# Kernel tuning notes

Hardware: AMD Instinct MI355X
Metric: run time of the kernel (lower is better)

## Reference

```python
import jax, jax.numpy as jnp
import numpy as np
from jax import lax

EPS = 1e-5
N_CROPS = 501
CROP_W = 500
RF = 65          # temporal receptive field
KS = 15          # conv1 kernel size
POOL = 3


def _bn(x, g, b, m, v, axis=1):
    shp = [1] * x.ndim
    shp[axis] = -1
    inv = g.reshape(shp) / jnp.sqrt(v.reshape(shp) + EPS)
    return (x - m.reshape(shp)) * inv + b.reshape(shp)


def setup_inputs() -> dict:
    key = jax.random.key(0)
    ks = jax.random.split(key, 16)
    B, C_IN, CH, T = 16, 1, 22, 1001
    F = 36
    OUT = 4
    FLAT = F * 43  # 1548 (corrected fc in_features; repo constant 504 is inconsistent)
    d = {
        "x": jax.random.normal(ks[0], (B, C_IN, CH, T), jnp.float32),
        # temporal conv [1,65]
        "w_t": jax.random.normal(ks[1], (F, 1, 1, RF), jnp.float32) * 0.1,
        "b_t": jax.random.normal(ks[2], (F,), jnp.float32) * 0.1,
        "bn_t_g": jax.random.uniform(ks[3], (F,), jnp.float32, 0.5, 1.5),
        "bn_t_b": jax.random.normal(ks[4], (F,), jnp.float32) * 0.1,
        "bn_t_m": jax.random.normal(ks[5], (F,), jnp.float32) * 0.1,
        "bn_t_v": jax.random.uniform(ks[6], (F,), jnp.float32, 0.5, 1.5),
        # spatial conv [22,1]
        "w_s": jax.random.normal(ks[7], (F, F, CH, 1), jnp.float32) * 0.05,
        "b_s": jax.random.normal(ks[8], (F,), jnp.float32) * 0.1,
        "bn_s_g": jax.random.uniform(ks[9], (F,), jnp.float32, 0.5, 1.5),
        "bn_s_b": jax.random.normal(ks[10], (F,), jnp.float32) * 0.1,
        "bn_s_m": jax.random.normal(ks[11], (F,), jnp.float32) * 0.1,
        "bn_s_v": jax.random.uniform(ks[12], (F,), jnp.float32, 0.5, 1.5),
        # conv1 [1,15] (as 1-D conv over time)
        "w_c": jax.random.normal(ks[13], (F, F, KS), jnp.float32) * 0.05,
        "b_c": jax.random.normal(ks[14], (F,), jnp.float32) * 0.1,
        "bn_c_g": jnp.ones((F,), jnp.float32),
        "bn_c_b": jnp.zeros((F,), jnp.float32),
        "bn_c_m": jnp.zeros((F,), jnp.float32),
        "bn_c_v": jnp.ones((F,), jnp.float32),
        # fc
        "w_fc": jax.random.normal(ks[15], (OUT, FLAT), jnp.float32) * 0.02,
        "b_fc": jnp.zeros((OUT,), jnp.float32),
    }
    return d


def reference(x, w_t, b_t, bn_t_g, bn_t_b, bn_t_m, bn_t_v,
              w_s, b_s, bn_s_g, bn_s_b, bn_s_m, bn_s_v,
              w_c, b_c, bn_c_g, bn_c_b, bn_c_m, bn_c_v,
              w_fc, b_fc):
    B = x.shape[0]
    F = w_t.shape[0]
    OUT = b_fc.shape[0]

    # temporal + spatial conv/BN/ELU are shift-invariant -> compute once over full T
    h = lax.conv_general_dilated(x, w_t, (1, 1), 'VALID',
                                 dimension_numbers=('NCHW', 'OIHW', 'NCHW'))
    h = h + b_t[None, :, None, None]                       # [B,36,22,937]
    h = jax.nn.elu(_bn(h, bn_t_g, bn_t_b, bn_t_m, bn_t_v))
    h = lax.conv_general_dilated(h, w_s, (1, 1), 'VALID',
                                 dimension_numbers=('NCHW', 'OIHW', 'NCHW'))
    h = h + b_s[None, :, None, None]                       # [B,36,1,937]
    h = jax.nn.elu(_bn(h, bn_s_g, bn_s_b, bn_s_m, bn_s_v))
    h = h[:, :, 0, :]                                      # [B,36,937]

    TW = CROP_W - RF + 1  # 436: temporal width of each crop after temporal conv

    def crop_logits(i):
        sl = lax.dynamic_slice_in_dim(h, i, TW, axis=2)    # [B,36,436]
        p1 = sl[:, :, :435].reshape(B, F, 145, POOL).mean(-1)  # avgpool1 -> [B,36,145]
        c = lax.conv_general_dilated(p1, w_c, (1,), 'VALID',
                                     dimension_numbers=('NCH', 'OIH', 'NCH'))
        c = c + b_c[None, :, None]                          # [B,36,131]
        c = jax.nn.elu(_bn(c, bn_c_g, bn_c_b, bn_c_m, bn_c_v))
        p2 = c[:, :, :129].reshape(B, F, 43, POOL).mean(-1)  # avgpool2 -> [B,36,43]
        flat = p2.reshape(B, -1)                            # [B,1548]
        return flat @ w_fc.T + b_fc                         # [B,OUT]

    def step(acc, i):
        return acc + crop_logits(i), None

    init = jnp.zeros((B, OUT), x.dtype)
    total, _ = lax.scan(step, init, jnp.arange(N_CROPS))
    return total / N_CROPS
```

## Files before the change

### kernel.cpp

```cpp
#include <hip/hip_runtime.h>

#define EPS 1e-5f
#define B 16
#define CH 22
#define T_IN 1001
#define F 36
#define RF 65
#define T1 937
#define FC 792
#define KW 99
#define UN 885
#define PSPAN 304
#define KS 15
#define GN 295
#define WN 129
#define M43 43
#define BF 576
#define FLAT 1548

#define H2_OFF  0
#define EP_OFF  539712
#define WTT_OFF 4617792
#define WST_OFF 4620132
#define WCT_OFF 4648644
#define BN_OFF  4668084
#define H1_OFF  4668352

__device__ __forceinline__ float elu_f(float v) {
    return v > 0.f ? v : (__expf(v) - 1.f);
}

__global__ __launch_bounds__(256) void k_prep(
    const float* __restrict__ w_t, const float* __restrict__ w_s,
    const float* __restrict__ w_c,
    const float* __restrict__ b_t, const float* __restrict__ g_t,
    const float* __restrict__ be_t,const float* __restrict__ m_t,
    const float* __restrict__ v_t,
    const float* __restrict__ b_s, const float* __restrict__ g_s,
    const float* __restrict__ be_s,const float* __restrict__ m_s,
    const float* __restrict__ v_s,
    const float* __restrict__ b_c, const float* __restrict__ g_c,
    const float* __restrict__ be_c,const float* __restrict__ m_c,
    const float* __restrict__ v_c, const float* __restrict__ b_fc,
    float* __restrict__ wtT, float* __restrict__ wsT,
    float* __restrict__ wcT, float* __restrict__ bnz,
    float* __restrict__ out)
{
    int i = blockIdx.x * 256 + threadIdx.x;
    if (i < F * RF)     { int k = i / F,  fi = i % F; wtT[i] = w_t[fi * RF + k]; }
    if (i < FC * F)     { int fc = i / F, fo = i % F; wsT[i] = w_s[fo * FC + fc]; }
    if (i < F * KS * F) { int fk = i / F, fo = i % F; int f = fk / KS, k = fk % KS;
                          wcT[i] = w_c[(fo * F + f) * KS + k]; }
    if (i < F) {
        float s1 = g_t[i] * rsqrtf(v_t[i] + EPS);
        bnz[i]          = s1;
        bnz[F + i]      = (b_t[i] - m_t[i]) * s1 + be_t[i];
        float s2 = g_s[i] * rsqrtf(v_s[i] + EPS);
        bnz[2 * F + i]  = s2;
        bnz[3 * F + i]  = (b_s[i] - m_s[i]) * s2 + be_s[i];
        float s3 = g_c[i] * rsqrtf(v_c[i] + EPS);
        bnz[4 * F + i]  = s3;
        bnz[5 * F + i]  = (b_c[i] - m_c[i]) * s3 + be_c[i];
    }
    if (i < B * 4) out[i] = b_fc[i & 3];
}

__global__ __launch_bounds__(256) void k_tconv(
    const float* __restrict__ x, const float* __restrict__ wtT,
    const float* __restrict__ bnz, float* __restrict__ h1,
    int t_base, int TS, int TSeff)
{
    const int tloc = blockIdx.x * 256 + threadIdx.x;
    const int b = blockIdx.z, ch = blockIdx.y;
    int t = t_base + tloc;
    int tc = t < (T1 - 1) ? t : (T1 - 1);
    const float* xp = x + (b * CH + ch) * T_IN + tc;

    float acc[F];
    #pragma unroll
    for (int j = 0; j < F; ++j) acc[j] = 0.f;

    #pragma unroll 4
    for (int kk = 0; kk < 16; ++kk) {
        float4 xv4 = *(const float4*)(xp + 4 * kk);
        const float* wr0 = wtT + (4 * kk + 0) * F;
        const float* wr1 = wtT + (4 * kk + 1) * F;
        const float* wr2 = wtT + (4 * kk + 2) * F;
        const float* wr3 = wtT + (4 * kk + 3) * F;
        #pragma unroll
        for (int j = 0; j < F; ++j) {
            acc[j] += xv4.x * wr0[j];
            acc[j] += xv4.y * wr1[j];
            acc[j] += xv4.z * wr2[j];
            acc[j] += xv4.w * wr3[j];
        }
    }
    {
        float xv = xp[64];
        const float* wr = wtT + 64 * F;
        #pragma unroll
        for (int j = 0; j < F; ++j) acc[j] += xv * wr[j];
    }

    if (t < T1 && tloc < TSeff) {
        #pragma unroll
        for (int j = 0; j < F; ++j) {
            float s1 = bnz[j], o1 = bnz[F + j];
            h1[((size_t)(b * F + j) * CH + ch) * TS + tloc] =
                elu_f(acc[j] * s1 + o1);
        }
    }
}

__global__ __launch_bounds__(512) void k_sconv(
    const float* __restrict__ h1, const float* __restrict__ wsT,
    const float* __restrict__ bnz, float* __restrict__ h2,
    int t_base, int TS, int TSeff)
{
    __shared__ float Ls[8 * F * 64];
    const int tid = threadIdx.x;
    const int lane = tid & 63;
    const int w = __builtin_amdgcn_readfirstlane(tid >> 6);
    const int b = blockIdx.y;
    const int tl0 = blockIdx.x * 64;
    int tl = tl0 + lane;
    int tlc = tl < (TSeff - 1) ? tl : (TSeff - 1);

    const float* hq = h1 + ((size_t)b * FC + w * KW) * TS + tlc;
    const float* wb = wsT + (w * KW) * F;

    float acc[F];
    #pragma unroll
    for (int j = 0; j < F; ++j) acc[j] = 0.f;

    #pragma unroll 11
    for (int fc = 0; fc < KW; ++fc) {
        float hv = hq[(size_t)fc * TS];
        const float* wr = wb + fc * F;
        #pragma unroll
        for (int j = 0; j < F; ++j) acc[j] += hv * wr[j];
    }

    #pragma unroll
    for (int j = 0; j < F; ++j) Ls[(w * F + j) * 64 + lane] = acc[j];
    __syncthreads();

    for (int i = tid; i < F * 64; i += 512) {
        float s = 0.f;
        #pragma unroll
        for (int wq = 0; wq < 8; ++wq) s += Ls[wq * (F * 64) + i];
        int fo = i >> 6;
        int tloc2 = tl0 + (i & 63);
        int tg = t_base + tloc2;
        if (tloc2 < TSeff) {
            float s2 = bnz[2 * F + fo], o2 = bnz[3 * F + fo];
            h2[(b * F + fo) * T1 + tg] = elu_f(s * s2 + o2);
        }
    }
}

__global__ __launch_bounds__(256) void k_qconv(
    const float* __restrict__ h2, const float* __restrict__ wcT,
    float* __restrict__ Ep)
{
    __shared__ float Ps[5 * PSPAN];
    const int tid = threadIdx.x;
    const int slice = blockIdx.y, b = blockIdx.z;
    const int u0 = blockIdx.x * 256;
    const int f_base = slice < 4 ? slice * 5 : 20 + (slice - 4) * 4;
    const int nf     = slice < 4 ? 5 : 4;

    for (int i = tid; i < nf * PSPAN; i += 256) {
        int fl = i / PSPAN, j = i % PSPAN;
        const float* hr = h2 + (size_t)(b * F + f_base + fl) * T1;
        int s = u0 + j;
        int s0 = s     < T1 - 1 ? s     : T1 - 1;
        int s1 = s + 1 < T1 - 1 ? s + 1 : T1 - 1;
        int s2 = s + 2 < T1 - 1 ? s + 2 : T1 - 1;
        Ps[i] = (hr[s0] + hr[s1] + hr[s2]) * (1.f / 3.f);
    }
    __syncthreads();

    const int lu = tid;

    float acc[F];
    #pragma unroll
    for (int j = 0; j < F; ++j) acc[j] = 0.f;

    for (int fl = 0; fl < nf; ++fl) {
        const int pb = fl * PSPAN + lu;
        #pragma unroll 5
        for (int k = 0; k < KS; ++k) {
            float pv = Ps[pb + 3 * k];
            const float* wr = wcT + ((f_base + fl) * KS + k) * F;
            #pragma unroll
            for (int j = 0; j < F; ++j) acc[j] += pv * wr[j];
        }
    }

    int u_g = u0 + lu;
    if (u_g < UN) {
        #pragma unroll
        for (int j = 0; j < F; ++j)
            Ep[(((size_t)slice * B + b) * F + j) * UN + u_g] = acc[j];
    }
}

__global__ __launch_bounds__(256) void k_wins(
    const float* __restrict__ Ep, const float* __restrict__ bnz,
    const float* __restrict__ w_fc, float* __restrict__ out)
{
    __shared__ float Es[UN];
    __shared__ float G[GN];
    __shared__ float Ws[WN];
    __shared__ float Sm[M43];
    const int tid = threadIdx.x;
    const int bf = blockIdx.x;
    const int b = bf / F, f = bf % F;
    const float sc = bnz[4 * F + f];
    const float oc = bnz[5 * F + f];
    for (int i = tid; i < UN; i += 256) {
        float s = 0.f;
        #pragma unroll
        for (int sl = 0; sl < 8; ++sl)
            s += Ep[((size_t)sl * BF + bf) * UN + i];
        Es[i] = elu_f(s * sc + oc);
    }
    __syncthreads();
    for (int q = tid; q < GN; q += 256)
        G[q] = Es[3 * q] + Es[3 * q + 1] + Es[3 * q + 2];
    __syncthreads();
    if (tid < WN) {
        float a = 0.f;
        for (int q = tid; q < tid + 167; ++q) a += G[q];
        Ws[tid] = a;
    }
    __syncthreads();
    if (tid < M43)
        Sm[tid] = (Ws[3 * tid] + Ws[3 * tid + 1] + Ws[3 * tid + 2]) * (1.f / 3.f);
    __syncthreads();
    if (tid < 4) {
        const float* wr = w_fc + tid * FLAT + f * M43;
        float a = 0.f;
        #pragma unroll 43
        for (int m = 0; m < M43; ++m) a += Sm[m] * wr[m];
        atomicAdd(&out[b * 4 + tid], a * (1.f / 501.f));
    }
}

extern "C" void kernel_launch(void* const* d_in, const int* in_sizes, int n_in,
                              void* d_out, int out_size, void* d_ws, size_t ws_size,
                              hipStream_t stream) {
    const float* x    = (const float*)d_in[0];
    const float* w_t  = (const float*)d_in[1];
    const float* b_t  = (const float*)d_in[2];
    const float* g_t  = (const float*)d_in[3];
    const float* be_t = (const float*)d_in[4];
    const float* m_t  = (const float*)d_in[5];
    const float* v_t  = (const float*)d_in[6];
    const float* w_s  = (const float*)d_in[7];
    const float* b_s  = (const float*)d_in[8];
    const float* g_s  = (const float*)d_in[9];
    const float* be_s = (const float*)d_in[10];
    const float* m_s  = (const float*)d_in[11];
    const float* v_s  = (const float*)d_in[12];
    const float* w_c  = (const float*)d_in[13];
    const float* b_c  = (const float*)d_in[14];
    const float* g_c  = (const float*)d_in[15];
    const float* be_c = (const float*)d_in[16];
    const float* m_c  = (const float*)d_in[17];
    const float* v_c  = (const float*)d_in[18];
    const float* w_fc = (const float*)d_in[19];
    const float* b_fc = (const float*)d_in[20];

    float* ws  = (float*)d_ws;
    float* h2  = ws + H2_OFF;
    float* Ep  = ws + EP_OFF;
    float* wtT = ws + WTT_OFF;
    float* wsT = ws + WST_OFF;
    float* wcT = ws + WCT_OFF;
    float* bnz = ws + BN_OFF;
    float* h1  = ws + H1_OFF;
    float* out = (float*)d_out;

    long long availF = (long long)(ws_size / 4) - (long long)H1_OFF;
    long long tsl = availF / (B * FC);
    int TS;
    if (tsl >= T1) TS = T1;
    else { TS = (int)(tsl & ~63LL); if (TS < 64) TS = 64; }
    int nslab = (T1 + TS - 1) / TS;

    k_prep<<<dim3(112), 256, 0, stream>>>(
        w_t, w_s, w_c, b_t, g_t, be_t, m_t, v_t,
        b_s, g_s, be_s, m_s, v_s, b_c, g_c, be_c, m_c, v_c, b_fc,
        wtT, wsT, wcT, bnz, out);

    for (int sl = 0; sl < nslab; ++sl) {
        int t_base = sl * TS;
        int TSeff = T1 - t_base; if (TSeff > TS) TSeff = TS;
        k_tconv<<<dim3((TSeff + 255) / 256, CH, B), 256, 0, stream>>>(
            x, wtT, bnz, h1, t_base, TS, TSeff);
        k_sconv<<<dim3((TSeff + 63) / 64, B), 512, 0, stream>>>(
            h1, wsT, bnz, h2, t_base, TS, TSeff);
    }

    k_qconv<<<dim3(4, 8, B), 256, 0, stream>>>(h2, wcT, Ep);
    k_wins<<<dim3(BF), 256, 0, stream>>>(Ep, bnz, w_fc, out);
}
```

Before: 176.4 us.

## Store temporal-conv intermediate as fp16 and split qconv by output channel

```diff
diff --git a/kernel.cpp b/kernel.cpp
--- a/kernel.cpp
+++ b/kernel.cpp
@@ -1,4 +1,5 @@
 #include <hip/hip_runtime.h>
+#include <hip/hip_fp16.h>
 
 #define EPS 1e-5f
 #define B 16
@@ -19,12 +20,12 @@
 #define FLAT 1548
 
 #define H2_OFF  0
-#define EP_OFF  539712
-#define WTT_OFF 4617792
-#define WST_OFF 4620132
-#define WCT_OFF 4648644
-#define BN_OFF  4668084
-#define H1_OFF  4668352
+#define E_OFF   539712
+#define WTT_OFF 1049472
+#define WST_OFF 1051812
+#define WCP_OFF 1080324
+#define BN_OFF  1101924
+#define H1_OFF  1102144
 
 __device__ __forceinline__ float elu_f(float v) {
     return v > 0.f ? v : (__expf(v) - 1.f);
@@ -43,14 +44,18 @@
     const float* __restrict__ be_c,const float* __restrict__ m_c,
     const float* __restrict__ v_c, const float* __restrict__ b_fc,
     float* __restrict__ wtT, float* __restrict__ wsT,
-    float* __restrict__ wcT, float* __restrict__ bnz,
+    float* __restrict__ wcP, float* __restrict__ bnz,
     float* __restrict__ out)
 {
     int i = blockIdx.x * 256 + threadIdx.x;
     if (i < F * RF)     { int k = i / F,  fi = i % F; wtT[i] = w_t[fi * RF + k]; }
     if (i < FC * F)     { int fc = i / F, fo = i % F; wsT[i] = w_s[fo * FC + fc]; }
-    if (i < F * KS * F) { int fk = i / F, fo = i % F; int f = fk / KS, k = fk % KS;
-                          wcT[i] = w_c[(fo * F + f) * KS + k]; }
+    if (i < 8 * F * KS * 5) {
+        int jj = i % 5, k = (i / 5) % KS, f = (i / (5 * KS)) % F, g = i / (5 * KS * F);
+        int fo = (g < 4 ? 5 * g : 20 + 4 * (g - 4)) + jj;
+        if (fo > F - 1) fo = F - 1;
+        wcP[i] = w_c[((size_t)fo * F + f) * KS + k];
+    }
     if (i < F) {
         float s1 = g_t[i] * rsqrtf(v_t[i] + EPS);
         bnz[i]          = s1;
@@ -67,7 +72,7 @@
 
 __global__ __launch_bounds__(256) void k_tconv(
     const float* __restrict__ x, const float* __restrict__ wtT,
-    const float* __restrict__ bnz, float* __restrict__ h1,
+    const float* __restrict__ bnz, __half* __restrict__ h1,
     int t_base, int TS, int TSeff)
 {
     const int tloc = blockIdx.x * 256 + threadIdx.x;
@@ -107,13 +112,13 @@
         for (int j = 0; j < F; ++j) {
             float s1 = bnz[j], o1 = bnz[F + j];
             h1[((size_t)(b * F + j) * CH + ch) * TS + tloc] =
-                elu_f(acc[j] * s1 + o1);
+                __float2half(elu_f(acc[j] * s1 + o1));
         }
     }
 }
 
 __global__ __launch_bounds__(512) void k_sconv(
-    const float* __restrict__ h1, const float* __restrict__ wsT,
+    const __half* __restrict__ h1, const float* __restrict__ wsT,
     const float* __restrict__ bnz, float* __restrict__ h2,
     int t_base, int TS, int TSeff)
 {
@@ -126,7 +131,7 @@
     int tl = tl0 + lane;
     int tlc = tl < (TSeff - 1) ? tl : (TSeff - 1);
 
-    const float* hq = h1 + ((size_t)b * FC + w * KW) * TS + tlc;
+    const __half* hq = h1 + ((size_t)b * FC + w * KW) * TS + tlc;
     const float* wb = wsT + (w * KW) * F;
 
     float acc[F];
@@ -135,7 +140,7 @@
 
     #pragma unroll 11
     for (int fc = 0; fc < KW; ++fc) {
-        float hv = hq[(size_t)fc * TS];
+        float hv = __half2float(hq[(size_t)fc * TS]);
         const float* wr = wb + fc * F;
         #pragma unroll
         for (int j = 0; j < F; ++j) acc[j] += hv * wr[j];
@@ -160,19 +165,19 @@
 }
 
 __global__ __launch_bounds__(256) void k_qconv(
-    const float* __restrict__ h2, const float* __restrict__ wcT,
-    float* __restrict__ Ep)
-{
-    __shared__ float Ps[5 * PSPAN];
+    const float* __restrict__ h2, const float* __restrict__ wcP,
+    const float* __restrict__ bnz, float* __restrict__ E)
+{
+    __shared__ float Ps[F * PSPAN];
     const int tid = threadIdx.x;
-    const int slice = blockIdx.y, b = blockIdx.z;
+    const int g = blockIdx.y, b = blockIdx.z;
     const int u0 = blockIdx.x * 256;
-    const int f_base = slice < 4 ? slice * 5 : 20 + (slice - 4) * 4;
-    const int nf     = slice < 4 ? 5 : 4;
-
-    for (int i = tid; i < nf * PSPAN; i += 256) {
+    const int fo0 = g < 4 ? g * 5 : 20 + (g - 4) * 4;
+    const int nfo = g < 4 ? 5 : 4;
+
+    for (int i = tid; i < F * PSPAN; i += 256) {
         int fl = i / PSPAN, j = i % PSPAN;
-        const float* hr = h2 + (size_t)(b * F + f_base + fl) * T1;
+        const float* hr = h2 + (size_t)(b * F + fl) * T1;
         int s = u0 + j;
         int s0 = s     < T1 - 1 ? s     : T1 - 1;
         int s1 = s + 1 < T1 - 1 ? s + 1 : T1 - 1;
@@ -181,34 +186,38 @@
     }
     __syncthreads();
 
-    const int lu = tid;
-
-    float acc[F];
+    float acc[5];
     #pragma unroll
-    for (int j = 0; j < F; ++j) acc[j] = 0.f;
-
-    for (int fl = 0; fl < nf; ++fl) {
-        const int pb = fl * PSPAN + lu;
+    for (int jj = 0; jj < 5; ++jj) acc[jj] = 0.f;
+
+    for (int f = 0; f < F; ++f) {
+        const int pb = f * PSPAN + tid;
+        const float* wf = wcP + (size_t)(g * F + f) * (KS * 5);
         #pragma unroll 5
         for (int k = 0; k < KS; ++k) {
             float pv = Ps[pb + 3 * k];
-            const float* wr = wcT + ((f_base + fl) * KS + k) * F;
+            const float* wr = wf + k * 5;
             #pragma unroll
-            for (int j = 0; j < F; ++j) acc[j] += pv * wr[j];
-        }
-    }
-
-    int u_g = u0 + lu;
+            for (int jj = 0; jj < 5; ++jj) acc[jj] += pv * wr[jj];
+        }
+    }
+
+    int u_g = u0 + tid;
     if (u_g < UN) {
         #pragma unroll
-        for (int j = 0; j < F; ++j)
-            Ep[(((size_t)slice * B + b) * F + j) * UN + u_g] = acc[j];
+        for (int jj = 0; jj < 5; ++jj) {
+            if (jj < nfo) {
+                int fo = fo0 + jj;
+                float sc = bnz[4 * F + fo], oc = bnz[5 * F + fo];
+                E[(size_t)(b * F + fo) * UN + u_g] = elu_f(acc[jj] * sc + oc);
+            }
+        }
     }
 }
 
 __global__ __launch_bounds__(256) void k_wins(
-    const float* __restrict__ Ep, const float* __restrict__ bnz,
-    const float* __restrict__ w_fc, float* __restrict__ out)
+    const float* __restrict__ E, const float* __restrict__ w_fc,
+    float* __restrict__ out)
 {
     __shared__ float Es[UN];
     __shared__ float G[GN];
@@ -217,15 +226,8 @@
     const int tid = threadIdx.x;
     const int bf = blockIdx.x;
     const int b = bf / F, f = bf % F;
-    const float sc = bnz[4 * F + f];
-    const float oc = bnz[5 * F + f];
-    for (int i = tid; i < UN; i += 256) {
-        float s = 0.f;
-        #pragma unroll
-        for (int sl = 0; sl < 8; ++sl)
-            s += Ep[((size_t)sl * BF + bf) * UN + i];
-        Es[i] = elu_f(s * sc + oc);
-    }
+    const float* er = E + (size_t)bf * UN;
+    for (int i = tid; i < UN; i += 256) Es[i] = er[i];
     __syncthreads();
     for (int q = tid; q < GN; q += 256)
         G[q] = Es[3 * q] + Es[3 * q + 1] + Es[3 * q + 2];
@@ -275,16 +277,16 @@
 
     float* ws  = (float*)d_ws;
     float* h2  = ws + H2_OFF;
-    float* Ep  = ws + EP_OFF;
+    float* E   = ws + E_OFF;
     float* wtT = ws + WTT_OFF;
     float* wsT = ws + WST_OFF;
-    float* wcT = ws + WCT_OFF;
+    float* wcP = ws + WCP_OFF;
     float* bnz = ws + BN_OFF;
-    float* h1  = ws + H1_OFF;
+    __half* h1 = (__half*)(ws + H1_OFF);
     float* out = (float*)d_out;
 
-    long long availF = (long long)(ws_size / 4) - (long long)H1_OFF;
-    long long tsl = availF / (B * FC);
+    long long availH = ((long long)(ws_size / 4) - (long long)H1_OFF) * 2;
+    long long tsl = availH / (B * FC);
     int TS;
     if (tsl >= T1) TS = T1;
     else { TS = (int)(tsl & ~63LL); if (TS < 64) TS = 64; }
@@ -293,7 +295,7 @@
     k_prep<<<dim3(112), 256, 0, stream>>>(
         w_t, w_s, w_c, b_t, g_t, be_t, m_t, v_t,
         b_s, g_s, be_s, m_s, v_s, b_c, g_c, be_c, m_c, v_c, b_fc,
-        wtT, wsT, wcT, bnz, out);
+        wtT, wsT, wcP, bnz, out);
 
     for (int sl = 0; sl < nslab; ++sl) {
         int t_base = sl * TS;
@@ -304,6 +306,6 @@
             h1, wsT, bnz, h2, t_base, TS, TSeff);
     }
 
-    k_qconv<<<dim3(4, 8, B), 256, 0, stream>>>(h2, wcT, Ep);
-    k_wins<<<dim3(BF), 256, 0, stream>>>(Ep, bnz, w_fc, out);
-}
+    k_qconv<<<dim3(4, 8, B), 256, 0, stream>>>(h2, wcP, bnz, E);
+    k_wins<<<dim3(BF), 256, 0, stream>>>(E, w_fc, out);
+}
```

Result: slower. 200.3 us (+13.5%).

## Split temporal conv reduction across two waves and halve sconv LDS buffer

Applied to the files above, without the earlier changes.

```diff
diff --git a/kernel.cpp b/kernel.cpp
--- a/kernel.cpp
+++ b/kernel.cpp
@@ -65,28 +65,34 @@
     if (i < B * 4) out[i] = b_fc[i & 3];
 }
 
-__global__ __launch_bounds__(256) void k_tconv(
+__global__ __launch_bounds__(512) void k_tconv(
     const float* __restrict__ x, const float* __restrict__ wtT,
     const float* __restrict__ bnz, float* __restrict__ h1,
     int t_base, int TS, int TSeff)
 {
-    const int tloc = blockIdx.x * 256 + threadIdx.x;
+    __shared__ float Ls[4 * F * 64];
+    const int tid = threadIdx.x;
+    const int lane = tid & 63;
+    const int w = __builtin_amdgcn_readfirstlane(tid >> 6);
+    const int tsub = w & 3, khalf = w >> 2;
     const int b = blockIdx.z, ch = blockIdx.y;
-    int t = t_base + tloc;
+    const int tl0 = blockIdx.x * 256 + tsub * 64;
+    int t = t_base + tl0 + lane;
     int tc = t < (T1 - 1) ? t : (T1 - 1);
     const float* xp = x + (b * CH + ch) * T_IN + tc;
+    const int k0 = khalf * 32;
 
     float acc[F];
     #pragma unroll
     for (int j = 0; j < F; ++j) acc[j] = 0.f;
 
     #pragma unroll 4
-    for (int kk = 0; kk < 16; ++kk) {
-        float4 xv4 = *(const float4*)(xp + 4 * kk);
-        const float* wr0 = wtT + (4 * kk + 0) * F;
-        const float* wr1 = wtT + (4 * kk + 1) * F;
-        const float* wr2 = wtT + (4 * kk + 2) * F;
-        const float* wr3 = wtT + (4 * kk + 3) * F;
+    for (int kk = 0; kk < 8; ++kk) {
+        float4 xv4 = *(const float4*)(xp + k0 + 4 * kk);
+        const float* wr0 = wtT + (k0 + 4 * kk + 0) * F;
+        const float* wr1 = wtT + (k0 + 4 * kk + 1) * F;
+        const float* wr2 = wtT + (k0 + 4 * kk + 2) * F;
+        const float* wr3 = wtT + (k0 + 4 * kk + 3) * F;
         #pragma unroll
         for (int j = 0; j < F; ++j) {
             acc[j] += xv4.x * wr0[j];
@@ -95,19 +101,35 @@
             acc[j] += xv4.w * wr3[j];
         }
     }
-    {
+    if (khalf == 1) {
         float xv = xp[64];
         const float* wr = wtT + 64 * F;
         #pragma unroll
         for (int j = 0; j < F; ++j) acc[j] += xv * wr[j];
     }
 
-    if (t < T1 && tloc < TSeff) {
-        #pragma unroll
-        for (int j = 0; j < F; ++j) {
-            float s1 = bnz[j], o1 = bnz[F + j];
-            h1[((size_t)(b * F + j) * CH + ch) * TS + tloc] =
-                elu_f(acc[j] * s1 + o1);
+    float* row = &Ls[(size_t)tsub * (F * 64)];
+    if (khalf == 0) {
+        #pragma unroll
+        for (int j = 0; j < F; ++j) row[j * 64 + lane] = acc[j];
+    }
+    __syncthreads();
+    if (khalf == 1) {
+        #pragma unroll
+        for (int j = 0; j < F; ++j) row[j * 64 + lane] += acc[j];
+    }
+    __syncthreads();
+
+    for (int i = tid; i < 4 * F * 64; i += 512) {
+        int l2 = i & 63;
+        int fo = (i >> 6) % F;
+        int ts2 = i / (F * 64);
+        int tloc = blockIdx.x * 256 + ts2 * 64 + l2;
+        int tg = t_base + tloc;
+        if (tloc < TSeff && tg < T1) {
+            float s1 = bnz[fo], o1 = bnz[F + fo];
+            h1[((size_t)(b * F + fo) * CH + ch) * TS + tloc] =
+                elu_f(Ls[i] * s1 + o1);
         }
     }
 }
@@ -117,7 +139,7 @@
     const float* __restrict__ bnz, float* __restrict__ h2,
     int t_base, int TS, int TSeff)
 {
-    __shared__ float Ls[8 * F * 64];
+    __shared__ float Ls[4 * F * 64];
     const int tid = threadIdx.x;
     const int lane = tid & 63;
     const int w = __builtin_amdgcn_readfirstlane(tid >> 6);
@@ -141,14 +163,20 @@
         for (int j = 0; j < F; ++j) acc[j] += hv * wr[j];
     }
 
-    #pragma unroll
-    for (int j = 0; j < F; ++j) Ls[(w * F + j) * 64 + lane] = acc[j];
+    float* row = &Ls[(size_t)(w & 3) * (F * 64)];
+    if (w < 4) {
+        #pragma unroll
+        for (int j = 0; j < F; ++j) row[j * 64 + lane] = acc[j];
+    }
+    __syncthreads();
+    if (w >= 4) {
+        #pragma unroll
+        for (int j = 0; j < F; ++j) row[j * 64 + lane] += acc[j];
+    }
     __syncthreads();
 
     for (int i = tid; i < F * 64; i += 512) {
-        float s = 0.f;
-        #pragma unroll
-        for (int wq = 0; wq < 8; ++wq) s += Ls[wq * (F * 64) + i];
+        float s = Ls[i] + Ls[F * 64 + i] + Ls[2 * F * 64 + i] + Ls[3 * F * 64 + i];
         int fo = i >> 6;
         int tloc2 = tl0 + (i & 63);
         int tg = t_base + tloc2;
@@ -298,7 +326,7 @@
     for (int sl = 0; sl < nslab; ++sl) {
         int t_base = sl * TS;
         int TSeff = T1 - t_base; if (TSeff > TS) TSeff = TS;
-        k_tconv<<<dim3((TSeff + 255) / 256, CH, B), 256, 0, stream>>>(
+        k_tconv<<<dim3((TSeff + 255) / 256, CH, B), 512, 0, stream>>>(
             x, wtT, bnz, h1, t_base, TS, TSeff);
         k_sconv<<<dim3((TSeff + 63) / 64, B), 512, 0, stream>>>(
             h1, wsT, bnz, h2, t_base, TS, TSeff);
```

Measured after the change: 189.5 us. 7.4% more time.
